# Kernel optimization log

Measured on AMD Instinct MI355X. Metric: run time of the kernel, lower is better.

Reference implementation:

```python
import jax, jax.numpy as jnp
from jax import lax
import numpy as np

B = 8192   # samples
L = 32     # predicted chars per sample (num_chars[i])
M = 32     # target labels per sample (num_labels[i])
C = 96     # character classes


def _edit_trace(pred, tgt):
    """Levenshtein DP + backtrace for one sample.
    pred: [L] int, tgt: [M] int.
    Returns (ti, tj, valid) of length L+M: 1-based (i,j) positions of the
    diagonal (match/substitute) moves on the optimal edit path, as emitted by
    distance_and_trace; valid masks non-diagonal / out-of-path steps."""
    Ls, Ms = pred.shape[0], tgt.shape[0]
    cost = (pred[:, None] != tgt[None, :]).astype(jnp.int32)  # [L,M]
    row0 = jnp.arange(Ms + 1, dtype=jnp.int32)

    def row_step(prev, crow):
        first = prev[0] + 1
        def col_step(left, z):
            up, diag, c = z
            v = jnp.minimum(jnp.minimum(up + 1, left + 1), diag + c)
            return v, v
        _, rest = lax.scan(col_step, first, (prev[1:], prev[:-1], crow))
        new = jnp.concatenate([first[None], rest])
        return new, new

    _, rows = lax.scan(row_step, row0, cost)
    D = jnp.concatenate([row0[None, :], rows], axis=0)  # [L+1, M+1]

    def bt_step(carry, _):
        i, j = carry
        c = cost[jnp.maximum(i - 1, 0), jnp.maximum(j - 1, 0)]
        dij = D[i, j]
        diag = (i > 0) & (j > 0) & (D[i - 1, j - 1] + c == dij)
        up = (~diag) & (i > 0) & (D[i - 1, j] + 1 == dij)
        left = (~diag) & (~up) & (j > 0)
        ni = i - (diag | up).astype(jnp.int32)
        nj = j - (diag | left).astype(jnp.int32)
        return (ni, nj), (i, j, diag)

    (_, _), (ti, tj, valid) = lax.scan(
        bt_step, (jnp.int32(Ls), jnp.int32(Ms)), None, length=Ls + Ms)
    return ti, tj, valid


def _forward(x, y, num_chars, num_labels):
    b = num_chars.shape[0]
    c = x.shape[1]
    l = x.shape[0] // b
    m = y.shape[0] // b
    logits = x.reshape(b, l, c)          # [B,L,C]
    labels = y.reshape(b, m)             # [B,M]
    pred = jnp.argmax(logits, axis=-1)   # torch.max(x,1) indices
    ti, tj, valid = jax.vmap(_edit_trace)(pred, labels)  # [B, L+M] each
    logp = jax.nn.log_softmax(logits, axis=-1)
    xi = jnp.where(valid, ti - 1, 0)     # trace[:,0]-1 (+ per-sample offset via reshape)
    yi = jnp.where(valid, tj - 1, 0)     # trace[:,1]-1
    lab = jnp.take_along_axis(labels, yi, axis=1)                 # [B,L+M]
    lp = jnp.take_along_axis(logp, xi[..., None], axis=1)         # [B,L+M,C]
    ce = -jnp.take_along_axis(lp, lab[..., None], axis=2)[..., 0]  # [B,L+M]
    cnt = valid.sum(axis=1)
    per_sample = jnp.where(valid, ce, 0.0).sum(axis=1) / jnp.maximum(cnt, 1)
    nonempty = cnt > 0                   # attenuation: skip empty traces
    total = jnp.where(nonempty, per_sample, 0.0).sum()
    return total / nonempty.sum()


def setup_inputs() -> dict:
    key = jax.random.key(0)
    k1, k2 = jax.random.split(key)
    x = jax.random.normal(k1, (B * L, C), dtype=jnp.float32)
    y = jax.random.randint(k2, (B * M,), 0, C, dtype=jnp.int32)
    num_chars = jnp.full((B,), L, dtype=jnp.int32)
    num_labels = jnp.full((B,), M, dtype=jnp.int32)
    return {"x": x, "y": y, "num_chars": num_chars, "num_labels": num_labels}


def reference(x, y, num_chars, num_labels):
    return _forward(x, y, num_chars, num_labels)
```

## Files before the change

### kernel.cpp

```cpp
#include <hip/hip_runtime.h>
#include <stdint.h>

#define BNUM  8192
#define LROWS 32
#define MLAB  32
#define CCLS  96
#define SPB   4
#define NBLK  (BNUM/SPB)
#define XFL   (LROWS*CCLS)
#define SFL   (XFL + 2*LROWS)

typedef float f32x4 __attribute__((ext_vector_type(4)));

__device__ __forceinline__ int dpp_wshr1_i32(int v) {
    return __builtin_amdgcn_update_dpp(0, v, 0x138, 0xF, 0xF, true);
}
__device__ __forceinline__ float dpp_wshr1_f32(float v) {
    return __int_as_float(
        __builtin_amdgcn_update_dpp(0, __float_as_int(v), 0x138, 0xF, 0xF, true));
}

__device__ __forceinline__ int swz12(int k, int r) {
    return (k < 8) ? (k ^ (r & 7)) : (8 + ((k - 8) ^ (r & 3)));
}

__device__ __forceinline__ void gload16(const float* g, float* l) {
    __builtin_amdgcn_global_load_lds(
        (const __attribute__((address_space(1))) unsigned int*)g,
        (__attribute__((address_space(3))) unsigned int*)l,
        16, 0, 0);
}

__global__ __launch_bounds__(256, 3) void editloss_main(
    const float* __restrict__ x, const int* __restrict__ y,
    float* __restrict__ partial_sum, float* __restrict__ partial_cnt)
{
    __shared__ float S[SPB * SFL];

    const int tid  = threadIdx.x;
    const int w    = tid >> 6;
    const int lane = tid & 63;
    const int r    = lane & 31;
    const int h    = lane >> 5;

    const int    sb = blockIdx.x * SPB + w;
    const float* gx = x + (size_t)sb * XFL;
    float*       Sw = &S[w * SFL];

#pragma unroll
    for (int t = 0; t < 12; ++t) {
        const int q   = t * 64 + lane;
        const int rr  = (q * 683) >> 14;
        const int rem = q - rr * 24;
        const int hh  = (rem >= 12) ? 1 : 0;
        const int kp  = rem - 12 * hh;
        const int kk  = swz12(kp, rr);
        const int G   = rr * 24 + 12 * hh + kk;
        gload16(gx + G * 4, Sw + t * 256);
    }
    asm volatile("s_waitcnt vmcnt(0)" ::: "memory");

    {
        f32x4 va[12];
#pragma unroll
        for (int k = 0; k < 12; ++k) {
            const int p = r * 24 + h * 12 + swz12(k, r);
            va[k] = *(const f32x4*)(Sw + p * 4);
        }
        float bmA = -1e30f, bmB = -1e30f; int biA = 0, biB = 0;
        float bsA = 0.f, bsB = 0.f;
#pragma unroll
        for (int k = 0; k < 12; ++k) {
            const f32x4 v = va[k];
            const int base = h * 48 + k * 4;
            if (k < 6) {
                if (v[0] > bmA) { bmA = v[0]; biA = base + 0; }
                if (v[1] > bmA) { bmA = v[1]; biA = base + 1; }
                if (v[2] > bmA) { bmA = v[2]; biA = base + 2; }
                if (v[3] > bmA) { bmA = v[3]; biA = base + 3; }
                bsA += __expf(v[0]) + __expf(v[1]) + __expf(v[2]) + __expf(v[3]);
            } else {
                if (v[0] > bmB) { bmB = v[0]; biB = base + 0; }
                if (v[1] > bmB) { bmB = v[1]; biB = base + 1; }
                if (v[2] > bmB) { bmB = v[2]; biB = base + 2; }
                if (v[3] > bmB) { bmB = v[3]; biB = base + 3; }
                bsB += __expf(v[0]) + __expf(v[1]) + __expf(v[2]) + __expf(v[3]);
            }
        }
        float mL = bmA; int iL = biA;
        if (bmB > mL) { mL = bmB; iL = biB; }
        const float sL = bsA + bsB;
        const float mP = __shfl_xor(mL, 32);
        const int   iP = __shfl_xor(iL, 32);
        const float sP = __shfl_xor(sL, 32);
        const float mLo = h ? mP : mL;  const int iLo = h ? iP : iL;
        const float mHi = h ? mL : mP;  const int iHi = h ? iL : iP;
        const float sLo = h ? sP : sL;  const float sHi = h ? sL : sP;
        float m = mLo; int idx = iLo;
        if (mHi > m) { m = mHi; idx = iHi; }
        const float lse = __logf(sLo + sHi);
        if (h == 0) {
            Sw[XFL + r * 2 + 0] = lse;
            Sw[XFL + r * 2 + 1] = (float)idx;
        }
    }
    __syncthreads();
    if (w >= 2) return;

    const int    sLoc = w * 2 + h;
    const int    samp = blockIdx.x * SPB + sLoc;
    float*       Sg   = &S[sLoc * SFL];
    const int    lab  = y[samp * MLAB + r];
    {
        const int   hh = (lab >= 48) ? 1 : 0;
        const int   kq = (lab - 48 * hh) >> 2;
        const int   el = lab & 3;
        const float fl = (float)lab;
#pragma unroll
        for (int rr = 0; rr < LROWS; ++rr) {
            const float lse = Sg[XFL + rr * 2 + 0];
            const float prf = Sg[XFL + rr * 2 + 1];
            const int   p   = rr * 24 + 12 * hh + swz12(kq, rr);
            const float xg  = Sg[p * 4 + el];
            const float ce  = lse - xg;
            Sg[rr * 96 + r] = (prf == fl) ? ce : -ce;
        }
    }
    asm volatile("s_waitcnt lgkmcnt(0)" ::: "memory");

    const int j = r + 1;
    int   prevW = 0;   float prevCE = 0.f;
    int   diagW = 0;   float diagCE = 0.f;
#pragma unroll 4
    for (int d = 1; d <= LROWS + MLAB; ++d) {
        const int   lWs  = dpp_wshr1_i32(prevW);
        const float lCEs = dpp_wshr1_f32(prevCE);
        const int i = d - j;
        const int   lW  = (r == 0) ? max(i, 0)     : lWs;
        const float lCE = (r == 0) ? 0.f           : lCEs;
        const int   dW  = (r == 0) ? max(i - 1, 0) : diagW;
        const float dCE = (r == 0) ? 0.f           : diagCE;
        int curW; float curCE;
        if (i <= 0) {
            curW = j; curCE = 0.f;
        } else if (i > LROWS) {
            curW = prevW; curCE = prevCE;
        } else {
            const int uD = prevW & 255, uC = prevW >> 8;
            const int lD = lW & 255,    lC = lW >> 8;
            const int dD = dW & 255,    dC = dW >> 8;
            const float ct  = Sg[(i - 1) * 96 + r];
            const int   c   = (ct < 0.f) ? 1 : 0;
            const int nD = min(min(uD, lD) + 1, dD + c);
            const bool dg = (dD + c == nD);
            const bool up = !dg && (uD + 1 == nD);
            int nC; float nCE;
            if (dg)      { nC = dC + 1; nCE = dCE + fabsf(ct); }
            else if (up) { nC = uC;     nCE = prevCE;          }
            else         { nC = lC;     nCE = lCE;             }
            curW = nD | (nC << 8);
            curCE = nCE;
        }
        diagW = lWs; diagCE = lCEs;
        prevW = curW; prevCE = curCE;
    }

    if (r == 31) {
        const int cnt = prevW >> 8;
        partial_sum[samp] = (cnt > 0) ? prevCE / (float)cnt : 0.f;
        partial_cnt[samp] = (cnt > 0) ? 1.f : 0.f;
    }
}

__global__ __launch_bounds__(256) void editloss_finalize(
    const float* __restrict__ partial_sum, const float* __restrict__ partial_cnt,
    float* __restrict__ out, int n)
{
    float s = 0.f, c = 0.f;
    for (int k = threadIdx.x; k < n; k += 256) {
        s += partial_sum[k];
        c += partial_cnt[k];
    }
#pragma unroll
    for (int d = 32; d >= 1; d >>= 1) {
        s += __shfl_xor(s, d);
        c += __shfl_xor(c, d);
    }
    __shared__ float ss[4], cc[4];
    const int w = threadIdx.x >> 6, lane = threadIdx.x & 63;
    if (lane == 0) { ss[w] = s; cc[w] = c; }
    __syncthreads();
    if (threadIdx.x == 0) {
        const float S  = ss[0] + ss[1] + ss[2] + ss[3];
        const float C2 = cc[0] + cc[1] + cc[2] + cc[3];
        out[0] = (C2 > 0.f) ? (S / C2) : 0.f;
    }
}

extern "C" void kernel_launch(void* const* d_in, const int* in_sizes, int n_in,
                              void* d_out, int out_size, void* d_ws, size_t ws_size,
                              hipStream_t stream) {
    const float* x = (const float*)d_in[0];
    const int*   y = (const int*)d_in[1];
    float* out = (float*)d_out;

    float* partial_sum = (float*)d_ws;
    float* partial_cnt = partial_sum + BNUM;

    editloss_main<<<NBLK, 256, 0, stream>>>(x, y, partial_sum, partial_cnt);
    editloss_finalize<<<1, 256, 0, stream>>>(partial_sum, partial_cnt, out, BNUM);
}
```

Measured before the change: 178.3 us.

## Use one 64-thread block per sample with direct global row loads

Switches from 256-thread blocks handling four samples (with LDS staging via global_load_lds and a block barrier) to one wavefront per sample. Each lane loads its logits row slice straight from global memory into registers, and the per-label gather is read from global instead of swizzled LDS. This removes the LDS staging, the __syncthreads, and the idle half-block during the DP. In exchange it launches four times as many small blocks, and both half-waves now run the DP for the same sample with redundant work. The gather becomes an uncoalesced global read, relying on the cache to hit.

```diff
diff --git a/kernel.cpp b/kernel.cpp
--- a/kernel.cpp
+++ b/kernel.cpp
@@ -5,10 +5,6 @@
 #define LROWS 32
 #define MLAB  32
 #define CCLS  96
-#define SPB   4
-#define NBLK  (BNUM/SPB)
-#define XFL   (LROWS*CCLS)
-#define SFL   (XFL + 2*LROWS)
 
 typedef float f32x4 __attribute__((ext_vector_type(4)));
 
@@ -20,53 +16,31 @@
         __builtin_amdgcn_update_dpp(0, __float_as_int(v), 0x138, 0xF, 0xF, true));
 }
 
-__device__ __forceinline__ int swz12(int k, int r) {
-    return (k < 8) ? (k ^ (r & 7)) : (8 + ((k - 8) ^ (r & 3)));
-}
-
-__device__ __forceinline__ void gload16(const float* g, float* l) {
-    __builtin_amdgcn_global_load_lds(
-        (const __attribute__((address_space(1))) unsigned int*)g,
-        (__attribute__((address_space(3))) unsigned int*)l,
-        16, 0, 0);
-}
-
-__global__ __launch_bounds__(256, 3) void editloss_main(
+__global__ __launch_bounds__(64, 4) void editloss_main(
     const float* __restrict__ x, const int* __restrict__ y,
     float* __restrict__ partial_sum, float* __restrict__ partial_cnt)
 {
-    __shared__ float S[SPB * SFL];
+    __shared__ float  ce[LROWS * MLAB];
+    __shared__ float2 lp[LROWS];
 
-    const int tid  = threadIdx.x;
-    const int w    = tid >> 6;
-    const int lane = tid & 63;
+    const int lane = threadIdx.x;
     const int r    = lane & 31;
     const int h    = lane >> 5;
 
-    const int    sb = blockIdx.x * SPB + w;
-    const float* gx = x + (size_t)sb * XFL;
-    float*       Sw = &S[w * SFL];
-
-#pragma unroll
-    for (int t = 0; t < 12; ++t) {
-        const int q   = t * 64 + lane;
-        const int rr  = (q * 683) >> 14;
-        const int rem = q - rr * 24;
-        const int hh  = (rem >= 12) ? 1 : 0;
-        const int kp  = rem - 12 * hh;
-        const int kk  = swz12(kp, rr);
-        const int G   = rr * 24 + 12 * hh + kk;
-        gload16(gx + G * 4, Sw + t * 256);
-    }
-    asm volatile("s_waitcnt vmcnt(0)" ::: "memory");
+    const int    sbm = blockIdx.x;
+    const float* gx  = x + (size_t)sbm * (LROWS * CCLS);
+    const int    lab = y[sbm * MLAB + r];
 
     {
+        const f32x4* rowv = (const f32x4*)(gx + r * CCLS + h * 48);
         f32x4 va[12];
 #pragma unroll
-        for (int k = 0; k < 12; ++k) {
-            const int p = r * 24 + h * 12 + swz12(k, r);
-            va[k] = *(const f32x4*)(Sw + p * 4);
-        }
+        for (int k = 0; k < 12; ++k) va[k] = rowv[k];
+        asm volatile("" :
+            "+v"(va[0]), "+v"(va[1]), "+v"(va[2]),  "+v"(va[3]),
+            "+v"(va[4]), "+v"(va[5]), "+v"(va[6]),  "+v"(va[7]),
+            "+v"(va[8]), "+v"(va[9]), "+v"(va[10]), "+v"(va[11]));
+
         float bmA = -1e30f, bmB = -1e30f; int biA = 0, biB = 0;
         float bsA = 0.f, bsB = 0.f;
 #pragma unroll
@@ -99,31 +73,19 @@
         float m = mLo; int idx = iLo;
         if (mHi > m) { m = mHi; idx = iHi; }
         const float lse = __logf(sLo + sHi);
-        if (h == 0) {
-            Sw[XFL + r * 2 + 0] = lse;
-            Sw[XFL + r * 2 + 1] = (float)idx;
-        }
+        if (h == 0) lp[r] = make_float2(lse, (float)idx);
     }
-    __syncthreads();
-    if (w >= 2) return;
+    asm volatile("s_waitcnt lgkmcnt(0)" ::: "memory");
 
-    const int    sLoc = w * 2 + h;
-    const int    samp = blockIdx.x * SPB + sLoc;
-    float*       Sg   = &S[sLoc * SFL];
-    const int    lab  = y[samp * MLAB + r];
     {
-        const int   hh = (lab >= 48) ? 1 : 0;
-        const int   kq = (lab - 48 * hh) >> 2;
-        const int   el = lab & 3;
-        const float fl = (float)lab;
+        const float  fl   = (float)lab;
+        const float* gcol = gx + lab;
 #pragma unroll
         for (int rr = 0; rr < LROWS; ++rr) {
-            const float lse = Sg[XFL + rr * 2 + 0];
-            const float prf = Sg[XFL + rr * 2 + 1];
-            const int   p   = rr * 24 + 12 * hh + swz12(kq, rr);
-            const float xg  = Sg[p * 4 + el];
-            const float ce  = lse - xg;
-            Sg[rr * 96 + r] = (prf == fl) ? ce : -ce;
+            const float2 l2 = lp[rr];
+            const float  xg = gcol[rr * CCLS];
+            const float  c  = l2.x - xg;
+            if (h == 0) ce[rr * MLAB + r] = (l2.y == fl) ? c : -c;
         }
     }
     asm volatile("s_waitcnt lgkmcnt(0)" ::: "memory");
@@ -149,7 +111,7 @@
             const int uD = prevW & 255, uC = prevW >> 8;
             const int lD = lW & 255,    lC = lW >> 8;
             const int dD = dW & 255,    dC = dW >> 8;
-            const float ct  = Sg[(i - 1) * 96 + r];
+            const float ct  = ce[(i - 1) * MLAB + r];
             const int   c   = (ct < 0.f) ? 1 : 0;
             const int nD = min(min(uD, lD) + 1, dD + c);
             const bool dg = (dD + c == nD);
@@ -165,10 +127,10 @@
         prevW = curW; prevCE = curCE;
     }
 
-    if (r == 31) {
+    if (lane == 31) {
         const int cnt = prevW >> 8;
-        partial_sum[samp] = (cnt > 0) ? prevCE / (float)cnt : 0.f;
-        partial_cnt[samp] = (cnt > 0) ? 1.f : 0.f;
+        partial_sum[sbm] = (cnt > 0) ? prevCE / (float)cnt : 0.f;
+        partial_cnt[sbm] = (cnt > 0) ? 1.f : 0.f;
     }
 }
 
@@ -207,6 +169,6 @@
     float* partial_sum = (float*)d_ws;
     float* partial_cnt = partial_sum + BNUM;
 
-    editloss_main<<<NBLK, 256, 0, stream>>>(x, y, partial_sum, partial_cnt);
+    editloss_main<<<BNUM, 64, 0, stream>>>(x, y, partial_sum, partial_cnt);
     editloss_finalize<<<1, 256, 0, stream>>>(partial_sum, partial_cnt, out, BNUM);
 }
```

New measurement: 169.9 us. 1.05x faster.
